# Optimization experiments

Hardware: AMD Instinct MI355X
Metric: run time of the kernel (lower is better)

The kernel has to match this reference:

```python
import jax, jax.numpy as jnp
import numpy as np

B, S, D_IN, D_OUT = 4, 2048, 1024, 1024


def setup_inputs() -> dict:
    key = jax.random.key(0)
    ks = jax.random.split(key, 7)
    s_in = 1.0 / np.sqrt(D_IN)
    return {
        "x": jax.random.normal(ks[0], (B, S, D_IN), dtype=jnp.float32),
        "Wq": jax.random.uniform(ks[1], (D_IN, D_OUT), jnp.float32, -s_in, s_in),
        "bq": jax.random.uniform(ks[2], (D_OUT,), jnp.float32, -s_in, s_in),
        "Wk": jax.random.uniform(ks[3], (D_IN, D_OUT), jnp.float32, -s_in, s_in),
        "bk": jax.random.uniform(ks[4], (D_OUT,), jnp.float32, -s_in, s_in),
        "Wv": jax.random.uniform(ks[5], (D_IN, D_OUT), jnp.float32, -s_in, s_in),
        "bv": jax.random.uniform(ks[6], (D_OUT,), jnp.float32, -s_in, s_in),
    }


def reference(x, Wq, bq, Wk, bk, Wv, bv):
    # q,k,v: [B, S, D_OUT]
    q = jnp.einsum("bsd,de->bse", x, Wq) + bq
    k = jnp.einsum("bsd,de->bse", x, Wk) + bk
    v = jnp.einsum("bsd,de->bse", x, Wv) + bv
    scale = 1.0 / jnp.sqrt(jnp.asarray(q.shape[-1], q.dtype))
    scores = jnp.einsum("bqe,bke->bqk", q, k) * scale  # [B, S, S]
    attn = jax.nn.softmax(scores, axis=-1)
    return jnp.einsum("bqk,bke->bqe", attn, v)
```

## Files before the change

### kernel.cpp

```cpp
#include <hip/hip_runtime.h>
#include <hip/hip_bf16.h>
#include <stdint.h>


#define Bsz 4
#define Ssz 2048
#define Dsz 1024

typedef __attribute__((ext_vector_type(8))) short short8;
typedef __attribute__((ext_vector_type(4))) float floatx4;
typedef const __attribute__((address_space(1))) void* gptr_t;
typedef __attribute__((address_space(3))) void* lptr_t;

__device__ __forceinline__ ushort f32_to_bf16(float f) {
    union { float f; uint32_t u; } c; c.f = f;
    uint32_t u = c.u;
    u += 0x7fffu + ((u >> 16) & 1u);
    return (ushort)(u >> 16);
}

template <bool OUT_BF16>
__device__ __forceinline__ void gemm128(
    const ushort* __restrict__ A, int lda,
    const ushort* __restrict__ Bt, int ldb,
    int K,
    void* __restrict__ Cout, int ldc,
    const float* __restrict__ bias, float alpha)
{
    __shared__ ushort lsA[128 * 32];
    __shared__ ushort lsB[128 * 32];

    const int tid  = threadIdx.x;
    const int row0 = blockIdx.y * 128;
    const int col0 = blockIdx.x * 128;

    const int lane = tid & 63;
    const int wave = tid >> 6;
    const int wr   = (wave >> 1) * 64;
    const int wc   = (wave & 1) * 64;
    const int m16  = lane & 15;
    const int quad = lane >> 4;

    floatx4 acc[4][4];
#pragma unroll
    for (int i = 0; i < 4; i++)
#pragma unroll
        for (int j = 0; j < 4; j++) acc[i][j] = (floatx4){0.f, 0.f, 0.f, 0.f};

    const ushort* ga = A  + (size_t)(row0 + (tid >> 2)) * lda + (tid & 3) * 8;
    const ushort* gb = Bt + (size_t)(col0 + (tid >> 2)) * ldb + (tid & 3) * 8;

    for (int k0 = 0; k0 < K; k0 += 32) {
        __syncthreads();
        __builtin_amdgcn_global_load_lds((gptr_t)(ga + k0),                     (lptr_t)(lsA + tid * 8),        16, 0, 0);
        __builtin_amdgcn_global_load_lds((gptr_t)(ga + k0 + (size_t)64 * lda), (lptr_t)(lsA + 2048 + tid * 8), 16, 0, 0);
        __builtin_amdgcn_global_load_lds((gptr_t)(gb + k0),                     (lptr_t)(lsB + tid * 8),        16, 0, 0);
        __builtin_amdgcn_global_load_lds((gptr_t)(gb + k0 + (size_t)64 * ldb), (lptr_t)(lsB + 2048 + tid * 8), 16, 0, 0);
        __syncthreads();

        short8 af[4], bfr[4];
#pragma unroll
        for (int mi = 0; mi < 4; mi++)
            af[mi] = *(const short8*)&lsA[(wr + mi * 16 + m16) * 32 + quad * 8];
#pragma unroll
        for (int ni = 0; ni < 4; ni++)
            bfr[ni] = *(const short8*)&lsB[(wc + ni * 16 + m16) * 32 + quad * 8];
#pragma unroll
        for (int mi = 0; mi < 4; mi++)
#pragma unroll
            for (int ni = 0; ni < 4; ni++)
                acc[mi][ni] = __builtin_amdgcn_mfma_f32_16x16x32_bf16(af[mi], bfr[ni], acc[mi][ni], 0, 0, 0);
    }

#pragma unroll
    for (int ni = 0; ni < 4; ni++) {
        const int gcol = col0 + wc + ni * 16 + m16;
        const float bv = bias ? bias[gcol] : 0.0f;
#pragma unroll
        for (int mi = 0; mi < 4; mi++) {
            const int grow0 = row0 + wr + mi * 16 + quad * 4;
#pragma unroll
            for (int j = 0; j < 4; j++) {
                float v = (acc[mi][ni][j] + bv) * alpha;
                if (OUT_BF16)
                    ((ushort*)Cout)[(size_t)(grow0 + j) * ldc + gcol] = f32_to_bf16(v);
                else
                    ((float*)Cout)[(size_t)(grow0 + j) * ldc + gcol] = v;
            }
        }
    }
}

__global__ __launch_bounds__(256) void k_cvt_x(const float* __restrict__ x, ushort* __restrict__ xb) {
    int i = (blockIdx.x * 256 + threadIdx.x) * 4;
    float4 v = *(const float4*)(x + i);
    ushort4 o;
    o.x = f32_to_bf16(v.x); o.y = f32_to_bf16(v.y);
    o.z = f32_to_bf16(v.z); o.w = f32_to_bf16(v.w);
    *(ushort4*)(xb + i) = o;
}

__global__ __launch_bounds__(256) void k_wt(const float* __restrict__ Wq, const float* __restrict__ Wk,
                                            const float* __restrict__ Wv, ushort* __restrict__ Wt) {
    __shared__ float tile[32][33];
    const int z = blockIdx.z;
    const float* W = (z == 0) ? Wq : ((z == 1) ? Wk : Wv);
    ushort* out = Wt + (size_t)z * Dsz * Dsz;
    const int kb = blockIdx.y * 32, nb = blockIdx.x * 32;
    const int tx = threadIdx.x, ty = threadIdx.y;
#pragma unroll
    for (int j = 0; j < 32; j += 8)
        tile[ty + j][tx] = W[(size_t)(kb + ty + j) * Dsz + nb + tx];
    __syncthreads();
#pragma unroll
    for (int j = 0; j < 32; j += 8)
        out[(size_t)(nb + ty + j) * Dsz + kb + tx] = f32_to_bf16(tile[tx][ty + j]);
}

__global__ __launch_bounds__(256) void k_qkv(const ushort* __restrict__ xb, const ushort* __restrict__ Wt,
                                             const float* __restrict__ bq, const float* __restrict__ bk,
                                             const float* __restrict__ bv, ushort* __restrict__ QKV) {
    const int z = blockIdx.z;
    const ushort* Bt = Wt + (size_t)z * Dsz * Dsz;
    const float* bias = (z == 0) ? bq : ((z == 1) ? bk : bv);
    ushort* out = QKV + (size_t)z * (Bsz * Ssz) * Dsz;
    const float alpha = (z == 0) ? 0.03125f : 1.0f;
    gemm128<true>(xb, Dsz, Bt, Dsz, Dsz, out, Dsz, bias, alpha);
}

__global__ __launch_bounds__(256) void k_scores(const ushort* __restrict__ QKV, float* __restrict__ scores) {
    const int b = blockIdx.z;
    const ushort* Q = QKV + (size_t)b * Ssz * Dsz;
    const ushort* Kb = QKV + (size_t)(Bsz + b) * Ssz * Dsz;
    gemm128<false>(Q, Dsz, Kb, Dsz, Dsz, scores + (size_t)b * Ssz * Ssz, Ssz, nullptr, 1.0f);
}

__global__ __launch_bounds__(256) void k_softmax(float* __restrict__ scores) {
    const size_t row = blockIdx.x;
    float* rp = scores + row * Ssz;
    const int tid = threadIdx.x;
    float vals[8];
    float m = -1e30f;
#pragma unroll
    for (int i = 0; i < 8; i++) { vals[i] = rp[tid + i * 256]; m = fmaxf(m, vals[i]); }
#pragma unroll
    for (int o = 32; o > 0; o >>= 1) m = fmaxf(m, __shfl_down(m, o, 64));
    __shared__ float redm[4];
    if ((tid & 63) == 0) redm[tid >> 6] = m;
    __syncthreads();
    const float rm = fmaxf(fmaxf(redm[0], redm[1]), fmaxf(redm[2], redm[3]));
    float s = 0.f;
#pragma unroll
    for (int i = 0; i < 8; i++) { vals[i] = __expf(vals[i] - rm); s += vals[i]; }
#pragma unroll
    for (int o = 32; o > 0; o >>= 1) s += __shfl_down(s, o, 64);
    __shared__ float reds[4];
    if ((tid & 63) == 0) reds[tid >> 6] = s;
    __syncthreads();
    const float inv = 1.0f / (reds[0] + reds[1] + reds[2] + reds[3]);
    ushort* op = (ushort*)rp;
#pragma unroll
    for (int i = 0; i < 8; i++) op[tid + i * 256] = f32_to_bf16(vals[i] * inv);
}

__global__ __launch_bounds__(256) void k_vt(const ushort* __restrict__ V, ushort* __restrict__ Vt) {
    __shared__ ushort tile[32][33];
    const int b = blockIdx.z;
    const ushort* Vb = V + (size_t)b * Ssz * Dsz;
    ushort* Vtb = Vt + (size_t)b * Dsz * Ssz;
    const int sb = blockIdx.y * 32, db = blockIdx.x * 32;
    const int tx = threadIdx.x, ty = threadIdx.y;
#pragma unroll
    for (int j = 0; j < 32; j += 8)
        tile[ty + j][tx] = Vb[(size_t)(sb + ty + j) * Dsz + db + tx];
    __syncthreads();
#pragma unroll
    for (int j = 0; j < 32; j += 8)
        Vtb[(size_t)(db + ty + j) * Ssz + sb + tx] = tile[tx][ty + j];
}

__global__ __launch_bounds__(256) void k_pv(const float* __restrict__ scores, const ushort* __restrict__ Vt,
                                            float* __restrict__ out) {
    const int b = blockIdx.z;
    const ushort* P = (const ushort*)(scores + (size_t)b * Ssz * Ssz);
    const ushort* Bt = Vt + (size_t)b * Dsz * Ssz;
    gemm128<false>(P, 2 * Ssz, Bt, Ssz, Ssz, out + (size_t)b * Ssz * Dsz, Dsz, nullptr, 1.0f);
}

extern "C" void kernel_launch(void* const* d_in, const int* in_sizes, int n_in,
                              void* d_out, int out_size, void* d_ws, size_t ws_size,
                              hipStream_t stream) {
    const float* x  = (const float*)d_in[0];
    const float* Wq = (const float*)d_in[1];
    const float* bq = (const float*)d_in[2];
    const float* Wk = (const float*)d_in[3];
    const float* bk = (const float*)d_in[4];
    const float* Wv = (const float*)d_in[5];
    const float* bv = (const float*)d_in[6];
    float* out = (float*)d_out;

    char* ws = (char*)d_ws;
    ushort* xb     = (ushort*)(ws);
    ushort* Wt     = (ushort*)(ws + 16777216);
    ushort* QKV    = (ushort*)(ws + 23068672);
    ushort* Vt     = (ushort*)(ws + 73400320);
    float*  scores = (float*) (ws + 90177536);

    k_cvt_x<<<dim3(Bsz * Ssz * Dsz / (256 * 4)), dim3(256), 0, stream>>>(x, xb);
    k_wt<<<dim3(32, 32, 3), dim3(32, 8), 0, stream>>>(Wq, Wk, Wv, Wt);
    k_qkv<<<dim3(Dsz / 128, Bsz * Ssz / 128, 3), dim3(256), 0, stream>>>(xb, Wt, bq, bk, bv, QKV);
    k_vt<<<dim3(Dsz / 32, Ssz / 32, Bsz), dim3(32, 8), 0, stream>>>(QKV + (size_t)2 * Bsz * Ssz * Dsz, Vt);
    k_scores<<<dim3(Ssz / 128, Ssz / 128, Bsz), dim3(256), 0, stream>>>(QKV, scores);
    k_softmax<<<dim3(Bsz * Ssz), dim3(256), 0, stream>>>(scores);
    k_pv<<<dim3(Dsz / 128, Ssz / 128, Bsz), dim3(256), 0, stream>>>(scores, Vt, out);
}
```

Baseline: 314.4 us.

## Enlarge GEMM tiles to 256x128 using 32x32x16 MFMA and vectorize softmax

Replaces the 128x128 GEMM tile with a 256x128 tile in which each wave computes 128x64 using 32x32x16 bf16 MFMA instructions. This raises arithmetic intensity per LDS load and halves the number of blocks. Launch bounds now request 2 blocks per CU, and softmax switches to float4 loads and ushort4 stores. The larger accumulator footprint raises register pressure, and the epilogue stores are still scattered, non-coalesced per-element writes.

After: 343.3 us. 9.2% more time.

```diff
diff --git a/kernel.cpp b/kernel.cpp
--- a/kernel.cpp
+++ b/kernel.cpp
@@ -8,7 +8,7 @@
 #define Dsz 1024
 
 typedef __attribute__((ext_vector_type(8))) short short8;
-typedef __attribute__((ext_vector_type(4))) float floatx4;
+typedef __attribute__((ext_vector_type(16))) float floatx16;
 typedef const __attribute__((address_space(1))) void* gptr_t;
 typedef __attribute__((address_space(3))) void* lptr_t;
 
@@ -20,72 +20,82 @@
 }
 
 template <bool OUT_BF16>
-__device__ __forceinline__ void gemm128(
+__device__ __forceinline__ void gemm256x128(
     const ushort* __restrict__ A, int lda,
     const ushort* __restrict__ Bt, int ldb,
     int K,
     void* __restrict__ Cout, int ldc,
     const float* __restrict__ bias, float alpha)
 {
-    __shared__ ushort lsA[128 * 32];
+    __shared__ ushort lsA[256 * 32];
     __shared__ ushort lsB[128 * 32];
 
     const int tid  = threadIdx.x;
-    const int row0 = blockIdx.y * 128;
+    const int row0 = blockIdx.y * 256;
     const int col0 = blockIdx.x * 128;
 
     const int lane = tid & 63;
     const int wave = tid >> 6;
-    const int wr   = (wave >> 1) * 64;
-    const int wc   = (wave & 1) * 64;
-    const int m16  = lane & 15;
-    const int quad = lane >> 4;
-
-    floatx4 acc[4][4];
+    const int wm   = (wave >> 1) * 128;
+    const int wn   = (wave & 1) * 64;
+    const int r32  = lane & 31;
+    const int half = lane >> 5;
+
+    floatx16 acc[4][2];
 #pragma unroll
     for (int i = 0; i < 4; i++)
 #pragma unroll
-        for (int j = 0; j < 4; j++) acc[i][j] = (floatx4){0.f, 0.f, 0.f, 0.f};
+        for (int j = 0; j < 2; j++)
+#pragma unroll
+            for (int r = 0; r < 16; r++) acc[i][j][r] = 0.f;
 
     const ushort* ga = A  + (size_t)(row0 + (tid >> 2)) * lda + (tid & 3) * 8;
     const ushort* gb = Bt + (size_t)(col0 + (tid >> 2)) * ldb + (tid & 3) * 8;
 
     for (int k0 = 0; k0 < K; k0 += 32) {
         __syncthreads();
-        __builtin_amdgcn_global_load_lds((gptr_t)(ga + k0),                     (lptr_t)(lsA + tid * 8),        16, 0, 0);
-        __builtin_amdgcn_global_load_lds((gptr_t)(ga + k0 + (size_t)64 * lda), (lptr_t)(lsA + 2048 + tid * 8), 16, 0, 0);
-        __builtin_amdgcn_global_load_lds((gptr_t)(gb + k0),                     (lptr_t)(lsB + tid * 8),        16, 0, 0);
-        __builtin_amdgcn_global_load_lds((gptr_t)(gb + k0 + (size_t)64 * ldb), (lptr_t)(lsB + 2048 + tid * 8), 16, 0, 0);
+#pragma unroll
+        for (int c = 0; c < 4; c++)
+            __builtin_amdgcn_global_load_lds((gptr_t)(ga + k0 + (size_t)(c * 64) * lda),
+                                             (lptr_t)(lsA + c * 2048 + tid * 8), 16, 0, 0);
+#pragma unroll
+        for (int c = 0; c < 2; c++)
+            __builtin_amdgcn_global_load_lds((gptr_t)(gb + k0 + (size_t)(c * 64) * ldb),
+                                             (lptr_t)(lsB + c * 2048 + tid * 8), 16, 0, 0);
         __syncthreads();
 
-        short8 af[4], bfr[4];
-#pragma unroll
-        for (int mi = 0; mi < 4; mi++)
-            af[mi] = *(const short8*)&lsA[(wr + mi * 16 + m16) * 32 + quad * 8];
-#pragma unroll
-        for (int ni = 0; ni < 4; ni++)
-            bfr[ni] = *(const short8*)&lsB[(wc + ni * 16 + m16) * 32 + quad * 8];
-#pragma unroll
-        for (int mi = 0; mi < 4; mi++)
-#pragma unroll
-            for (int ni = 0; ni < 4; ni++)
-                acc[mi][ni] = __builtin_amdgcn_mfma_f32_16x16x32_bf16(af[mi], bfr[ni], acc[mi][ni], 0, 0, 0);
+#pragma unroll
+        for (int ks = 0; ks < 2; ks++) {
+            short8 af[4], bf[2];
+#pragma unroll
+            for (int mi = 0; mi < 4; mi++)
+                af[mi] = *(const short8*)&lsA[(wm + mi * 32 + r32) * 32 + ks * 16 + half * 8];
+#pragma unroll
+            for (int ni = 0; ni < 2; ni++)
+                bf[ni] = *(const short8*)&lsB[(wn + ni * 32 + r32) * 32 + ks * 16 + half * 8];
+#pragma unroll
+            for (int mi = 0; mi < 4; mi++)
+#pragma unroll
+                for (int ni = 0; ni < 2; ni++)
+                    acc[mi][ni] = __builtin_amdgcn_mfma_f32_32x32x16_bf16(af[mi], bf[ni], acc[mi][ni], 0, 0, 0);
+        }
     }
 
 #pragma unroll
-    for (int ni = 0; ni < 4; ni++) {
-        const int gcol = col0 + wc + ni * 16 + m16;
+    for (int ni = 0; ni < 2; ni++) {
+        const int gcol = col0 + wn + ni * 32 + r32;
         const float bv = bias ? bias[gcol] : 0.0f;
 #pragma unroll
         for (int mi = 0; mi < 4; mi++) {
-            const int grow0 = row0 + wr + mi * 16 + quad * 4;
-#pragma unroll
-            for (int j = 0; j < 4; j++) {
-                float v = (acc[mi][ni][j] + bv) * alpha;
+            const int rbase = row0 + wm + mi * 32 + 4 * half;
+#pragma unroll
+            for (int r = 0; r < 16; r++) {
+                const int grow = rbase + (r & 3) + 8 * (r >> 2);
+                float v = (acc[mi][ni][r] + bv) * alpha;
                 if (OUT_BF16)
-                    ((ushort*)Cout)[(size_t)(grow0 + j) * ldc + gcol] = f32_to_bf16(v);
+                    ((ushort*)Cout)[(size_t)grow * ldc + gcol] = f32_to_bf16(v);
                 else
-                    ((float*)Cout)[(size_t)(grow0 + j) * ldc + gcol] = v;
+                    ((float*)Cout)[(size_t)grow * ldc + gcol] = v;
             }
         }
     }
@@ -117,50 +127,56 @@
         out[(size_t)(nb + ty + j) * Dsz + kb + tx] = f32_to_bf16(tile[tx][ty + j]);
 }
 
-__global__ __launch_bounds__(256) void k_qkv(const ushort* __restrict__ xb, const ushort* __restrict__ Wt,
-                                             const float* __restrict__ bq, const float* __restrict__ bk,
-                                             const float* __restrict__ bv, ushort* __restrict__ QKV) {
+__global__ __launch_bounds__(256, 2) void k_qkv(const ushort* __restrict__ xb, const ushort* __restrict__ Wt,
+                                                const float* __restrict__ bq, const float* __restrict__ bk,
+                                                const float* __restrict__ bv, ushort* __restrict__ QKV) {
     const int z = blockIdx.z;
     const ushort* Bt = Wt + (size_t)z * Dsz * Dsz;
     const float* bias = (z == 0) ? bq : ((z == 1) ? bk : bv);
     ushort* out = QKV + (size_t)z * (Bsz * Ssz) * Dsz;
     const float alpha = (z == 0) ? 0.03125f : 1.0f;
-    gemm128<true>(xb, Dsz, Bt, Dsz, Dsz, out, Dsz, bias, alpha);
-}
-
-__global__ __launch_bounds__(256) void k_scores(const ushort* __restrict__ QKV, float* __restrict__ scores) {
+    gemm256x128<true>(xb, Dsz, Bt, Dsz, Dsz, out, Dsz, bias, alpha);
+}
+
+__global__ __launch_bounds__(256, 2) void k_scores(const ushort* __restrict__ QKV, float* __restrict__ scores) {
     const int b = blockIdx.z;
     const ushort* Q = QKV + (size_t)b * Ssz * Dsz;
     const ushort* Kb = QKV + (size_t)(Bsz + b) * Ssz * Dsz;
-    gemm128<false>(Q, Dsz, Kb, Dsz, Dsz, scores + (size_t)b * Ssz * Ssz, Ssz, nullptr, 1.0f);
+    gemm256x128<false>(Q, Dsz, Kb, Dsz, Dsz, scores + (size_t)b * Ssz * Ssz, Ssz, nullptr, 1.0f);
 }
 
 __global__ __launch_bounds__(256) void k_softmax(float* __restrict__ scores) {
     const size_t row = blockIdx.x;
     float* rp = scores + row * Ssz;
     const int tid = threadIdx.x;
-    float vals[8];
-    float m = -1e30f;
-#pragma unroll
-    for (int i = 0; i < 8; i++) { vals[i] = rp[tid + i * 256]; m = fmaxf(m, vals[i]); }
+    float4 v0 = ((const float4*)rp)[tid];
+    float4 v1 = ((const float4*)rp)[tid + 256];
+    float m = fmaxf(fmaxf(fmaxf(v0.x, v0.y), fmaxf(v0.z, v0.w)),
+                    fmaxf(fmaxf(v1.x, v1.y), fmaxf(v1.z, v1.w)));
 #pragma unroll
     for (int o = 32; o > 0; o >>= 1) m = fmaxf(m, __shfl_down(m, o, 64));
     __shared__ float redm[4];
     if ((tid & 63) == 0) redm[tid >> 6] = m;
     __syncthreads();
     const float rm = fmaxf(fmaxf(redm[0], redm[1]), fmaxf(redm[2], redm[3]));
-    float s = 0.f;
-#pragma unroll
-    for (int i = 0; i < 8; i++) { vals[i] = __expf(vals[i] - rm); s += vals[i]; }
+    v0.x = __expf(v0.x - rm); v0.y = __expf(v0.y - rm);
+    v0.z = __expf(v0.z - rm); v0.w = __expf(v0.w - rm);
+    v1.x = __expf(v1.x - rm); v1.y = __expf(v1.y - rm);
+    v1.z = __expf(v1.z - rm); v1.w = __expf(v1.w - rm);
+    float s = v0.x + v0.y + v0.z + v0.w + v1.x + v1.y + v1.z + v1.w;
 #pragma unroll
     for (int o = 32; o > 0; o >>= 1) s += __shfl_down(s, o, 64);
     __shared__ float reds[4];
     if ((tid & 63) == 0) reds[tid >> 6] = s;
     __syncthreads();
     const float inv = 1.0f / (reds[0] + reds[1] + reds[2] + reds[3]);
-    ushort* op = (ushort*)rp;
-#pragma unroll
-    for (int i = 0; i < 8; i++) op[tid + i * 256] = f32_to_bf16(vals[i] * inv);
+    ushort4 o0, o1;
+    o0.x = f32_to_bf16(v0.x * inv); o0.y = f32_to_bf16(v0.y * inv);
+    o0.z = f32_to_bf16(v0.z * inv); o0.w = f32_to_bf16(v0.w * inv);
+    o1.x = f32_to_bf16(v1.x * inv); o1.y = f32_to_bf16(v1.y * inv);
+    o1.z = f32_to_bf16(v1.z * inv); o1.w = f32_to_bf16(v1.w * inv);
+    ((ushort4*)rp)[tid] = o0;
+    ((ushort4*)rp)[tid + 256] = o1;
 }
 
 __global__ __launch_bounds__(256) void k_vt(const ushort* __restrict__ V, ushort* __restrict__ Vt) {
@@ -179,12 +195,12 @@
         Vtb[(size_t)(db + ty + j) * Ssz + sb + tx] = tile[tx][ty + j];
 }
 
-__global__ __launch_bounds__(256) void k_pv(const float* __restrict__ scores, const ushort* __restrict__ Vt,
-                                            float* __restrict__ out) {
+__global__ __launch_bounds__(256, 2) void k_pv(const float* __restrict__ scores, const ushort* __restrict__ Vt,
+                                               float* __restrict__ out) {
     const int b = blockIdx.z;
     const ushort* P = (const ushort*)(scores + (size_t)b * Ssz * Ssz);
     const ushort* Bt = Vt + (size_t)b * Dsz * Ssz;
-    gemm128<false>(P, 2 * Ssz, Bt, Ssz, Ssz, out + (size_t)b * Ssz * Dsz, Dsz, nullptr, 1.0f);
+    gemm256x128<false>(P, 2 * Ssz, Bt, Ssz, Ssz, out + (size_t)b * Ssz * Dsz, Dsz, nullptr, 1.0f);
 }
 
 extern "C" void kernel_launch(void* const* d_in, const int* in_sizes, int n_in,
@@ -208,9 +224,9 @@
 
     k_cvt_x<<<dim3(Bsz * Ssz * Dsz / (256 * 4)), dim3(256), 0, stream>>>(x, xb);
     k_wt<<<dim3(32, 32, 3), dim3(32, 8), 0, stream>>>(Wq, Wk, Wv, Wt);
-    k_qkv<<<dim3(Dsz / 128, Bsz * Ssz / 128, 3), dim3(256), 0, stream>>>(xb, Wt, bq, bk, bv, QKV);
+    k_qkv<<<dim3(Dsz / 128, Bsz * Ssz / 256, 3), dim3(256), 0, stream>>>(xb, Wt, bq, bk, bv, QKV);
     k_vt<<<dim3(Dsz / 32, Ssz / 32, Bsz), dim3(32, 8), 0, stream>>>(QKV + (size_t)2 * Bsz * Ssz * Dsz, Vt);
-    k_scores<<<dim3(Ssz / 128, Ssz / 128, Bsz), dim3(256), 0, stream>>>(QKV, scores);
+    k_scores<<<dim3(Ssz / 128, Ssz / 256, Bsz), dim3(256), 0, stream>>>(QKV, scores);
     k_softmax<<<dim3(Bsz * Ssz), dim3(256), 0, stream>>>(scores);
-    k_pv<<<dim3(Dsz / 128, Ssz / 128, Bsz), dim3(256), 0, stream>>>(scores, Vt, out);
-}
+    k_pv<<<dim3(Dsz / 128, Ssz / 256, Bsz), dim3(256), 0, stream>>>(scores, Vt, out);
+}
```
